# Performance work log

Measured on AMD Instinct MI355X. Metric: run time of the kernel, lower is better.

The kernel has to match this reference:

```python
import jax, jax.numpy as jnp
import numpy as np

G, N_PER, P_EDGE = 128, 20, 0.2
INPUT_DIM, HIDDEN, OUT_DIM = 32, 64, 10


def _build_structures():
    rng = np.random.default_rng(0)
    n, g = N_PER, G
    A = rng.random((g, n, n)) < P_EDGE
    A = np.triu(A, 1)
    A = A | A.transpose(0, 2, 1)  # symmetric, zero diag
    gi, uu, vv = np.nonzero(A)
    edge_index = np.stack([uu + gi * n, vv + gi * n]).astype(np.int64)
    batch = np.repeat(np.arange(g), n).astype(np.int64)
    # ---- 2-sets ----
    iu, ju = np.triu_indices(n, 1)
    P2 = len(iu)
    M2 = np.zeros((n, n), np.int64)
    M2[iu, ju] = np.arange(P2); M2[ju, iu] = np.arange(P2)
    gu2 = (np.arange(g)[:, None] * n + iu[None]).ravel().astype(np.int64)
    gv2 = (np.arange(g)[:, None] * n + ju[None]).ravel().astype(np.int64)
    iso2 = A[:, iu, ju].astype(np.float32).reshape(-1, 1)
    w = np.arange(n)
    # branch A: (u,v) -> (v,w) if adj[v,w] & w!=u & adj[u,w]; branch B symmetric
    condA = A[:, ju, :] & A[:, iu, :] & (w[None, None, :] != iu[None, :, None])
    condB = A[:, iu, :] & A[:, ju, :] & (w[None, None, :] != ju[None, :, None])
    ga_, ia_, wa_ = np.nonzero(condA)
    gb_, ib_, wb_ = np.nonzero(condB)
    src2 = np.concatenate([ia_ + ga_ * P2, ib_ + gb_ * P2])
    dst2 = np.concatenate([M2[ju[ia_], wa_] + ga_ * P2, M2[iu[ib_], wb_] + gb_ * P2])
    two_edges = np.stack([src2, dst2]).astype(np.int64)
    two_batch = np.repeat(np.arange(g), P2).astype(np.int64)
    # ---- 3-sets ----
    trips = np.array([(a, b, c) for a in range(n) for b in range(a + 1, n) for c in range(b + 1, n)], np.int64)
    a, b, c = trips[:, 0], trips[:, 1], trips[:, 2]
    P3 = len(trips)
    M3 = np.zeros((n, n, n), np.int64)
    M3[a, b, c] = np.arange(P3)
    ga3 = (np.arange(g)[:, None] * n + a[None]).ravel().astype(np.int64)
    gb3 = (np.arange(g)[:, None] * n + b[None]).ravel().astype(np.int64)
    gc3 = (np.arange(g)[:, None] * n + c[None]).ravel().astype(np.int64)
    ec = A[:, a, b].astype(np.int64) + A[:, b, c].astype(np.int64) + A[:, a, c].astype(np.int64)
    iso3 = np.eye(4, dtype=np.float32)[ec.reshape(-1)]
    notin = (w[None] != a[:, None]) & (w[None] != b[:, None]) & (w[None] != c[:, None])  # [P3,n]
    srcs, dsts = [], []
    # branches: replace c (keep a,b), replace b (keep a,c), replace a (keep b,c)
    for k0, k1, nbr in ((a, b, c), (a, c, b), (b, c, a)):
        cond = A[:, nbr, :] & notin[None]
        gg_, ii_, dd_ = np.nonzero(cond)
        tri = np.sort(np.stack([k0[ii_], k1[ii_], dd_], 1), 1)
        srcs.append(ii_ + gg_ * P3)
        dsts.append(M3[tri[:, 0], tri[:, 1], tri[:, 2]] + gg_ * P3)
    three_edges = np.stack([np.concatenate(srcs), np.concatenate(dsts)]).astype(np.int64)
    three_batch = np.repeat(np.arange(g), P3).astype(np.int64)
    x = rng.standard_normal((g * n, INPUT_DIM)).astype(np.float32)
    return (x, edge_index, batch, gu2, gv2, iso2, two_edges, two_batch,
            ga3, gb3, gc3, iso3, three_edges, three_batch)


def setup_inputs() -> dict:
    (x, edge_index, batch, gu2, gv2, iso2, two_edges, two_batch,
     ga3, gb3, gc3, iso3, three_edges, three_batch) = _build_structures()
    rw = np.random.default_rng(1)
    def W(o, i):
        return jnp.asarray((rw.standard_normal((o, i)) * 0.1).astype(np.float32))
    H = HIDDEN
    return dict(
        x=jnp.asarray(x), edge_index=jnp.asarray(edge_index), batch=jnp.asarray(batch),
        gu2=jnp.asarray(gu2), gv2=jnp.asarray(gv2), iso2=jnp.asarray(iso2),
        two_edges=jnp.asarray(two_edges), two_batch=jnp.asarray(two_batch),
        ga3=jnp.asarray(ga3), gb3=jnp.asarray(gb3), gc3=jnp.asarray(gc3),
        iso3=jnp.asarray(iso3), three_edges=jnp.asarray(three_edges),
        three_batch=jnp.asarray(three_batch),
        g1W1_0=W(H, INPUT_DIM), g1W2_0=W(H, INPUT_DIM),
        g1W1_1=W(H, H), g1W2_1=W(H, H), g1W1_2=W(H, H), g1W2_2=W(H, H),
        g2W1_0=W(H, 2 * H + 1), g2W2_0=W(H, 2 * H + 1), g2W1_1=W(H, H), g2W2_1=W(H, H),
        g3W1_0=W(H, 3 * H + 4), g3W2_0=W(H, 3 * H + 4), g3W1_1=W(H, H), g3W2_1=W(H, H),
        cW1=W(H, 3 * H), cb1=jnp.zeros((H,), jnp.float32),
        cW2=W(OUT_DIM, H), cb2=jnp.zeros((OUT_DIM,), jnp.float32),
    )


def _layer(h, W1, W2, src, dst, num):
    # f(s) = relu(h W1^T + scatter_add(h W2^T gathered at src, dst))
    msg = (h @ W2.T)[src]  # project-then-gather; same math as gather-then-project
    nb = jax.ops.segment_sum(msg, dst, num_segments=num)
    return jax.nn.relu(h @ W1.T + nb)


def reference(x, edge_index, batch, gu2, gv2, iso2, two_edges, two_batch,
              ga3, gb3, gc3, iso3, three_edges, three_batch,
              g1W1_0, g1W2_0, g1W1_1, g1W2_1, g1W1_2, g1W2_2,
              g2W1_0, g2W2_0, g2W1_1, g2W2_1,
              g3W1_0, g3W2_0, g3W1_1, g3W2_1,
              cW1, cb1, cW2, cb2):
    N = x.shape[0]
    h = x
    for W1, W2 in ((g1W1_0, g1W2_0), (g1W1_1, g1W2_1), (g1W1_2, g1W2_2)):
        h = _layer(h, W1, W2, edge_index[0], edge_index[1], N)
    emb1 = jax.ops.segment_sum(h, batch, num_segments=G)
    h2 = jnp.concatenate([h[gu2], h[gv2], iso2], axis=1)
    n2 = h2.shape[0]
    for W1, W2 in ((g2W1_0, g2W2_0), (g2W1_1, g2W2_1)):
        h2 = _layer(h2, W1, W2, two_edges[0], two_edges[1], n2)
    emb2 = jax.ops.segment_sum(h2, two_batch, num_segments=G)
    h3 = jnp.concatenate([h[ga3], h[gb3], h[gc3], iso3], axis=1)
    n3 = h3.shape[0]
    for W1, W2 in ((g3W1_0, g3W2_0), (g3W1_1, g3W2_1)):
        h3 = _layer(h3, W1, W2, three_edges[0], three_edges[1], n3)
    emb3 = jax.ops.segment_sum(h3, three_batch, num_segments=G)
    comb = jnp.concatenate([emb1, emb2, emb3], axis=1)
    hid = jax.nn.relu(comb @ cW1.T + cb1)  # dropout is identity in eval mode
    return hid @ cW2.T + cb2
```

## Files before the change

kernel.cpp:

```cpp
#include <hip/hip_runtime.h>
#include <hip/hip_bf16.h>

#define HID 64
#define MROWS 1140
#define PAD1 20
#define PAD2 40
#define PAD3 60

typedef __hip_bfloat16  bf16;
typedef __hip_bfloat162 bf162;
typedef unsigned short  u16;
typedef __attribute__((ext_vector_type(8))) short bf8v;
typedef __attribute__((ext_vector_type(4))) float f4v;
typedef __attribute__((ext_vector_type(4))) unsigned int u4v;
__device__ __forceinline__ float bl(bf16 h) { return __bfloat162float(h); }

__global__ void zero_k(int* p, int n) {
    int i = blockIdx.x * 256 + threadIdx.x;
    if (i < n) p[i] = 0;
}

__global__ void fillp_k(const int* e1, int E1, int* c1, u16* s1, int p1, int P1_,
                        const int* e2, int E2, int* c2, u16* s2, int p2, int P2_,
                        const int* e3, int E3, int* c3, u16* s3, int p3, int P3_,
                        int nb1, int nb2) {
    int b = blockIdx.x;
    const int* edges; int E; int* cur; u16* csrc; int pad; int P; int lb;
    if (b < nb1)            { edges = e1; E = E1; cur = c1; csrc = s1; pad = p1; P = P1_; lb = b; }
    else if (b < nb1 + nb2) { edges = e2; E = E2; cur = c2; csrc = s2; pad = p2; P = P2_; lb = b - nb1; }
    else                    { edges = e3; E = E3; cur = c3; csrc = s3; pad = p3; P = P3_; lb = b - nb1 - nb2; }
    int e = lb * 256 + threadIdx.x;
    if (e >= E) return;
    int d = edges[E + e];
    int slot = atomicAdd(&cur[d], 1);
    if (slot < pad) csrc[(size_t)d * pad + slot] = (u16)(edges[e] % P);
}

struct FJob {
    const float *W1t, *W2t;
    const int *ga, *gb, *gc;
    const float *iso;
    const float *wc1, *wc2; int ldw, isoC, nT;
    const float *Wl1, *Wl2;
    const u16 *csrc; const int *cnt; int pad;
    bf16 *zc; bf16 *m1g;
    int P, ntiles, comboff;
};

__device__ __forceinline__ int msw(int row, int ch) {
    return (row << 6) + ((ch ^ (row & 7)) << 3);
}
__device__ __forceinline__ void accu4(u4v v, float* f) {
#pragma unroll
    for (int i = 0; i < 4; ++i) {
        f[2 * i]     += __uint_as_float(v[i] << 16);
        f[2 * i + 1] += __uint_as_float(v[i] & 0xffff0000u);
    }
}
__device__ __forceinline__ void accxy4(u4v v, float* zx, float* zy) {
#pragma unroll
    for (int i = 0; i < 4; ++i) {
        zx[i] += __uint_as_float(v[i] << 16);
        zy[i] += __uint_as_float(v[i] & 0xffff0000u);
    }
}
__device__ __forceinline__ bf8v pack8(const float* f) {
    bf16 tmp[8];
#pragma unroll
    for (int e = 0; e < 8; ++e) tmp[e] = __float2bfloat16(f[e]);
    bf8v r; __builtin_memcpy(&r, tmp, 16); return r;
}
__device__ __forceinline__ bf8v pack8relu(const float* f) {
    bf16 tmp[8];
#pragma unroll
    for (int e = 0; e < 8; ++e) tmp[e] = __float2bfloat16(fmaxf(f[e], 0.f));
    bf8v r; __builtin_memcpy(&r, tmp, 16); return r;
}
__device__ __forceinline__ u4v asu4(bf8v v) { u4v r; __builtin_memcpy(&r, &v, 16); return r; }
__device__ __forceinline__ void hsacc(const bf162* tb, int nd, int c4, float* zx, float* zy) {
    u4v v0 = *(const u4v*)(tb + (nd << 6) + (((c4    ) ^ (nd & 15)) << 2));
    u4v v1 = *(const u4v*)(tb + (nd << 6) + (((c4 + 1) ^ (nd & 15)) << 2));
    accxy4(v0, zx, zy);
    accxy4(v1, zx + 4, zy + 4);
}
__device__ __forceinline__ void hsaccY(const bf162* tb, int nd, int c4, float* zy) {
    u4v v0 = *(const u4v*)(tb + (nd << 6) + (((c4    ) ^ (nd & 15)) << 2));
    u4v v1 = *(const u4v*)(tb + (nd << 6) + (((c4 + 1) ^ (nd & 15)) << 2));
#pragma unroll
    for (int i = 0; i < 4; ++i) {
        zy[i]     += __uint_as_float(v0[i] & 0xffff0000u);
        zy[4 + i] += __uint_as_float(v1[i] & 0xffff0000u);
    }
}
__device__ __forceinline__ void naccum(const bf16* mL, int nbr, int quad, float* acc) {
    u4v v0 = *(const u4v*)(mL + msw(nbr, quad));
    u4v v1 = *(const u4v*)(mL + msw(nbr, quad + 4));
    accu4(v0, acc); accu4(v1, acc + 8);
}

__device__ __forceinline__ void run_k1(const FJob& jb, int g, int h,
                                       bf16* mLDS, bf16* wstage, const float* hb) {
    int t = threadIdx.x;
    const int P = jb.P, nT = jb.nT;
    const int gbase = g * P, nb20 = g * 20;
    int lane = t & 63, wv = t >> 6, quad = lane >> 4, m16 = lane & 15;

    bf162* hsA = (bf162*)wstage;
    const bf162* hsB = hsA + 1280;
    const bf162* hsC = hsA + 2560;
    bf16* mW = mLDS;
    for (int i = t; i < nT * 8192; i += 1024) {
        int table = i >> 13, r = i & 8191;
        int e = r & 7, mm = (r >> 3) & 15, qq = (r >> 7) & 3;
        int kk = (r >> 9) & 1, mat = (r >> 10) & 1, nn = r >> 11;
        const float* W = mat ? jb.W2t : jb.W1t;
        mW[i] = __float2bfloat16(W[(size_t)(nn * 16 + mm) * jb.ldw + table * 64 + kk * 32 + qq * 8 + e]);
    }
    float* wcT = (float*)(wstage + 7680);
    if (t < 512) {
        int mat = t >> 8, c = (t >> 6) & 3, f = t & 63;
        const float* W = mat ? jb.wc2 : jb.wc1;
        wcT[mat * 256 + c * 64 + f] = (c < jb.isoC) ? W[f * jb.ldw + c] : 0.f;
    }
    __syncthreads();
    if (wv < nT) {
        const bf16* mWt = mW + wv * 8192;
        bf8v a[2][2];
#pragma unroll
        for (int rt = 0; rt < 2; ++rt) {
            int node = rt * 16 + m16;
#pragma unroll
            for (int kt = 0; kt < 2; ++kt) {
                float tmp[8] = {0.f, 0.f, 0.f, 0.f, 0.f, 0.f, 0.f, 0.f};
                if (node < 20) {
                    const float* hr = hb + node * 65 + kt * 32 + quad * 8;
#pragma unroll
                    for (int e = 0; e < 8; ++e) tmp[e] = hr[e];
                }
                a[rt][kt] = pack8(tmp);
            }
        }
        bf162* hsT = hsA + wv * 1280;
#pragma unroll
        for (int n = 0; n < 4; ++n) {
            const bf8v b1k0 = *(const bf8v*)(mWt + ((((n*2+0)*2+0)*4+quad)*16+m16)*8);
            const bf8v b1k1 = *(const bf8v*)(mWt + ((((n*2+0)*2+1)*4+quad)*16+m16)*8);
            const bf8v b2k0 = *(const bf8v*)(mWt + ((((n*2+1)*2+0)*4+quad)*16+m16)*8);
            const bf8v b2k1 = *(const bf8v*)(mWt + ((((n*2+1)*2+1)*4+quad)*16+m16)*8);
#pragma unroll
            for (int rt = 0; rt < 2; ++rt) {
                f4v acca = {0.f, 0.f, 0.f, 0.f};
                f4v accb = {0.f, 0.f, 0.f, 0.f};
                acca = __builtin_amdgcn_mfma_f32_16x16x32_bf16(a[rt][0], b1k0, acca, 0, 0, 0);
                acca = __builtin_amdgcn_mfma_f32_16x16x32_bf16(a[rt][1], b1k1, acca, 0, 0, 0);
                accb = __builtin_amdgcn_mfma_f32_16x16x32_bf16(a[rt][0], b2k0, accb, 0, 0, 0);
                accb = __builtin_amdgcn_mfma_f32_16x16x32_bf16(a[rt][1], b2k1, accb, 0, 0, 0);
                int col = n * 16 + m16, c4 = col >> 2;
#pragma unroll
                for (int r = 0; r < 4; ++r) {
                    int node = rt * 16 + quad * 4 + r;
                    if (node < 20) {
                        bf162 v; v.x = __float2bfloat16(acca[r]); v.y = __float2bfloat16(accb[r]);
                        hsT[(node << 6) + ((c4 ^ (node & 15)) << 2) + (col & 3)] = v;
                    }
                }
            }
        }
    }
    __syncthreads();

    bf8v z8[3][2];
#pragma unroll
    for (int k = 0; k < 3; ++k) {
        int tile = wv + k * 16;
        if (tile >= jb.ntiles) continue;
#pragma unroll
        for (int rt = 0; rt < 2; ++rt) {
            bool own = (rt == h);
            int row = tile * 32 + rt * 16 + m16;
            float zx[16], zy[16];
#pragma unroll
            for (int j = 0; j < 16; ++j) { zx[j] = 0.f; zy[j] = 0.f; }
            if (row < P) {
                size_t gr = (size_t)gbase + row;
                int na = jb.ga[gr] - nb20;
                int nb = jb.gb[gr] - nb20;
                int nc = 0;
                const float* w1r; const float* w2r; float isw;
                if (nT == 3) {
                    nc = jb.gc[gr] - nb20;
                    float4 iv = ((const float4*)jb.iso)[gr];
                    int ec = (int)(iv.y + 2.f * iv.z + 3.f * iv.w + 0.5f);
                    w1r = wcT + ec * 64; w2r = wcT + 256 + ec * 64; isw = 1.f;
                } else {
                    w1r = wcT; w2r = wcT + 256; isw = jb.iso[gr];
                }
#pragma unroll
                for (int kt = 0; kt < 2; ++kt) {
                    int c4 = kt * 8 + quad * 2;
                    int f0 = kt * 32 + quad * 8;
                    if (own) {
                        hsacc(hsA, na, c4, zx + kt * 8, zy + kt * 8);
                        hsacc(hsB, nb, c4, zx + kt * 8, zy + kt * 8);
                        if (nT == 3) hsacc(hsC, nc, c4, zx + kt * 8, zy + kt * 8);
#pragma unroll
                        for (int e = 0; e < 8; ++e)
                            zx[kt * 8 + e] = fmaf(isw, w1r[f0 + e], zx[kt * 8 + e]);
                    } else {
                        hsaccY(hsA, na, c4, zy + kt * 8);
                        hsaccY(hsB, nb, c4, zy + kt * 8);
                        if (nT == 3) hsaccY(hsC, nc, c4, zy + kt * 8);
                    }
#pragma unroll
                    for (int e = 0; e < 8; ++e)
                        zy[kt * 8 + e] = fmaf(isw, w2r[f0 + e], zy[kt * 8 + e]);
                }
                *(bf8v*)(mLDS + msw(row, quad))     = pack8(zy);
                *(bf8v*)(mLDS + msw(row, quad + 4)) = pack8(zy + 8);
            }
            if (own) { z8[k][0] = pack8(zx); z8[k][1] = pack8(zx + 8); }
        }
    }
    __syncthreads();

    for (int i = t; i < 8192; i += 1024) {
        int e = i & 7, mm = (i >> 3) & 15, qq = (i >> 7) & 3;
        int kk = (i >> 9) & 1, mat = (i >> 10) & 1, nn = i >> 11;
        const float* W = mat ? jb.Wl2 : jb.Wl1;
        wstage[i] = __float2bfloat16(W[(nn * 16 + mm) * HID + kk * 32 + qq * 8 + e]);
    }
#pragma unroll
    for (int k = 0; k < 3; ++k) {
        int tile = wv + k * 16;
        if (tile >= jb.ntiles) continue;
        int row = tile * 32 + h * 16 + m16;
        float acc[16];
#pragma unroll
        for (int j = 0; j < 16; ++j) acc[j] = 0.f;
        accu4(asu4(z8[k][0]), acc);
        accu4(asu4(z8[k][1]), acc + 8);
        if (row < P) {
            size_t gr = (size_t)gbase + row;
            int cnt = jb.cnt[gr];
            const u16* cs = jb.csrc + gr * (size_t)jb.pad;
            int kk = 0;
            for (; kk + 4 <= cnt; kk += 4) {
                int n0 = cs[kk], n1 = cs[kk + 1], n2 = cs[kk + 2], n3 = cs[kk + 3];
                naccum(mLDS, n0, quad, acc); naccum(mLDS, n1, quad, acc);
                naccum(mLDS, n2, quad, acc); naccum(mLDS, n3, quad, acc);
            }
            for (; kk < cnt; ++kk) naccum(mLDS, cs[kk], quad, acc);
        }
        z8[k][0] = pack8relu(acc);
        z8[k][1] = pack8relu(acc + 8);
    }
    __syncthreads();

#pragma unroll
    for (int k = 0; k < 3; ++k) {
        int tile = wv + k * 16;
        if (tile >= jb.ntiles) continue;
        int j0 = tile * 32;
#pragma unroll
        for (int n = 0; n < 4; ++n) {
            const bf8v b1k0 = *(const bf8v*)(wstage + ((((n*2+0)*2+0)*4+quad)*16+m16)*8);
            const bf8v b1k1 = *(const bf8v*)(wstage + ((((n*2+0)*2+1)*4+quad)*16+m16)*8);
            const bf8v b2k0 = *(const bf8v*)(wstage + ((((n*2+1)*2+0)*4+quad)*16+m16)*8);
            const bf8v b2k1 = *(const bf8v*)(wstage + ((((n*2+1)*2+1)*4+quad)*16+m16)*8);
            f4v acca = {0.f, 0.f, 0.f, 0.f};
            f4v accb = {0.f, 0.f, 0.f, 0.f};
            acca = __builtin_amdgcn_mfma_f32_16x16x32_bf16(z8[k][0], b1k0, acca, 0, 0, 0);
            acca = __builtin_amdgcn_mfma_f32_16x16x32_bf16(z8[k][1], b1k1, acca, 0, 0, 0);
            accb = __builtin_amdgcn_mfma_f32_16x16x32_bf16(z8[k][0], b2k0, accb, 0, 0, 0);
            accb = __builtin_amdgcn_mfma_f32_16x16x32_bf16(z8[k][1], b2k1, accb, 0, 0, 0);
            int col = n * 16 + m16;
#pragma unroll
            for (int r = 0; r < 4; ++r) {
                int row = j0 + h * 16 + quad * 4 + r;
                if (row < P) {
                    jb.zc[((size_t)gbase + row) * HID + col]  = __float2bfloat16(acca[r]);
                    jb.m1g[((size_t)gbase + row) * HID + col] = __float2bfloat16(accb[r]);
                }
            }
        }
    }
}

__global__ __launch_bounds__(1024, 1)
void fused23a_k(const float* __restrict__ x,
                const int* __restrict__ cnt1, const u16* __restrict__ csrc1,
                const float* __restrict__ W10, const float* __restrict__ W20,
                const float* __restrict__ W11, const float* __restrict__ W21,
                const float* __restrict__ W12, const float* __restrict__ W22,
                FJob j3, FJob j2, float* __restrict__ comb, int G) {
    __shared__ __align__(16) bf16 mLDS[MROWS * HID];
    __shared__ __align__(16) bf16 wstage[8768];
    int b = blockIdx.x, t = threadIdx.x;
    int g = b >> 1, h = b & 1;
    if (h == 0 && t < 128) comb[g * 192 + 64 + t] = 0.f;

    float* hb = (float*)(mLDS + 70360);
    float* mb = (float*)(mLDS + 67800);
    float* zb = (float*)(mLDS + 65240);
    bf16* wf  = mLDS;
    int lane = t & 63, wv = t >> 6, quad = lane >> 4, m16 = lane & 15;
    int col = lane, r0 = wv;
    bool has2 = r0 < 4; int r1 = 16 + r0;
    if (t < 640) hb[(t >> 5) * 65 + (t & 31)] = x[(size_t)g * 640 + t];
    for (int i = t; i < 20480; i += 1024) {
        bf16 v;
        if (i < 4096) {
            int r = i;
            int e = r & 7, mm = (r >> 3) & 15, qq = (r >> 7) & 3;
            int mat = (r >> 9) & 1, nn = r >> 10;
            const float* W = mat ? W20 : W10;
            v = __float2bfloat16(W[(nn * 16 + mm) * 32 + qq * 8 + e]);
        } else {
            int j = i - 4096;
            int l2 = j >> 13, r = j & 8191;
            int e = r & 7, mm = (r >> 3) & 15, qq = (r >> 7) & 3;
            int kt = (r >> 9) & 1, mat = (r >> 10) & 1, nn = r >> 11;
            const float* W = l2 ? (mat ? W22 : W12) : (mat ? W21 : W11);
            v = __float2bfloat16(W[(nn * 16 + mm) * 64 + kt * 32 + qq * 8 + e]);
        }
        wf[i] = v;
    }
    __syncthreads();
#pragma unroll 1
    for (int l = 0; l < 3; ++l) {
        if (wv < 2) {
            const bf16* wbase = wf + (l == 0 ? 0 : (l == 1 ? 4096 : 12288));
            const int nK = l ? 2 : 1;
            const int lstep = l ? 2048 : 1024;
            const int mstep = l ? 1024 : 512;
            bf8v a[2][2];
#pragma unroll
            for (int rt = 0; rt < 2; ++rt) {
                int node = rt * 16 + m16;
#pragma unroll
                for (int kt = 0; kt < 2; ++kt) {
                    float tmp[8] = {0.f, 0.f, 0.f, 0.f, 0.f, 0.f, 0.f, 0.f};
                    if (node < 20 && kt < nK) {
                        const float* hr = hb + node * 65 + kt * 32 + quad * 8;
#pragma unroll
                        for (int e = 0; e < 8; ++e) tmp[e] = hr[e];
                    }
                    a[rt][kt] = pack8(tmp);
                }
            }
            float* ob = wv ? mb : zb;
#pragma unroll
            for (int n = 0; n < 4; ++n) {
                const bf16* bp = wbase + n * lstep + wv * mstep + (quad * 16 + m16) * 8;
                bf8v b0 = *(const bf8v*)bp;
                bf8v b1 = b0;
                if (l) b1 = *(const bf8v*)(bp + 512);
#pragma unroll
                for (int rt = 0; rt < 2; ++rt) {
                    f4v acc = {0.f, 0.f, 0.f, 0.f};
                    acc = __builtin_amdgcn_mfma_f32_16x16x32_bf16(a[rt][0], b0, acc, 0, 0, 0);
                    if (l) acc = __builtin_amdgcn_mfma_f32_16x16x32_bf16(a[rt][1], b1, acc, 0, 0, 0);
                    int c = n * 16 + m16;
#pragma unroll
                    for (int r = 0; r < 4; ++r) {
                        int row = rt * 16 + quad * 4 + r;
                        if (row < 20) ob[row * 64 + c] = acc[r];
                    }
                }
            }
        }
        __syncthreads();
        {
            float az = zb[r0 * 64 + col];
            int cnt = cnt1[g * 20 + r0];
            const u16* cs = csrc1 + (size_t)(g * 20 + r0) * PAD1;
            for (int k = 0; k < cnt; ++k) az += mb[cs[k] * 64 + col];
            hb[r0 * 65 + col] = fmaxf(az, 0.f);
        }
        if (has2) {
            float az = zb[r1 * 64 + col];
            int cnt = cnt1[g * 20 + r1];
            const u16* cs = csrc1 + (size_t)(g * 20 + r1) * PAD1;
            for (int k = 0; k < cnt; ++k) az += mb[cs[k] * 64 + col];
            hb[r1 * 65 + col] = fmaxf(az, 0.f);
        }
        __syncthreads();
    }
    if (h == 0 && t < 64) {
        float s = 0.f;
#pragma unroll
        for (int r = 0; r < 20; ++r) s += hb[r * 65 + t];
        comb[g * 192 + t] = s;
    }
    run_k1(j2, g, h, mLDS, wstage, hb);
    __syncthreads();
    run_k1(j3, g, h, mLDS, wstage, hb);
}

__device__ __forceinline__ void run_k2(const FJob& jb, int g, int h,
                                       bf16* mLDS, float* part, float* comb) {
    int t = threadIdx.x;
    const int P = jb.P;
    const int gbase = g * P;
    int lane = t & 63, wv = t >> 6, quad = lane >> 4, m16 = lane & 15;
    for (int i = t; i < P * 8; i += 1024) {
        int row = i >> 3, ch = i & 7;
        u4v v = *(const u4v*)(jb.m1g + ((size_t)gbase + row) * HID + ch * 8);
        *(u4v*)(mLDS + msw(row, ch)) = v;
    }
    __syncthreads();
    float ps[16];
#pragma unroll
    for (int j = 0; j < 16; ++j) ps[j] = 0.f;
#pragma unroll
    for (int k = 0; k < 3; ++k) {
        int tile = wv + k * 16;
        if (tile >= jb.ntiles) continue;
        int row = tile * 32 + h * 16 + m16;
        if (row < P) {
            float acc[16];
#pragma unroll
            for (int j = 0; j < 16; ++j) acc[j] = 0.f;
            size_t gr = (size_t)gbase + row;
            u4v zc0 = *(const u4v*)(jb.zc + gr * HID + quad * 8);
            u4v zc1 = *(const u4v*)(jb.zc + gr * HID + 32 + quad * 8);
            accu4(zc0, acc); accu4(zc1, acc + 8);
            int cnt = jb.cnt[gr];
            const u16* cs = jb.csrc + gr * (size_t)jb.pad;
            int kk = 0;
            for (; kk + 4 <= cnt; kk += 4) {
                int n0 = cs[kk], n1 = cs[kk + 1], n2 = cs[kk + 2], n3 = cs[kk + 3];
                naccum(mLDS, n0, quad, acc); naccum(mLDS, n1, quad, acc);
                naccum(mLDS, n2, quad, acc); naccum(mLDS, n3, quad, acc);
            }
            for (; kk < cnt; ++kk) naccum(mLDS, cs[kk], quad, acc);
#pragma unroll
            for (int j = 0; j < 16; ++j) ps[j] += fmaxf(acc[j], 0.f);
        }
    }
#pragma unroll
    for (int j = 0; j < 16; ++j) {
        ps[j] += __shfl_xor(ps[j], 1, 64);
        ps[j] += __shfl_xor(ps[j], 2, 64);
        ps[j] += __shfl_xor(ps[j], 4, 64);
        ps[j] += __shfl_xor(ps[j], 8, 64);
    }
    if (m16 == 0) {
#pragma unroll
        for (int kt = 0; kt < 2; ++kt)
#pragma unroll
            for (int e = 0; e < 8; ++e)
                part[wv * 64 + kt * 32 + quad * 8 + e] = ps[kt * 8 + e];
    }
    __syncthreads();
    if (t < 64) {
        float s = 0.f;
#pragma unroll
        for (int w = 0; w < 16; ++w) s += part[w * 64 + t];
        atomicAdd(&comb[g * 192 + jb.comboff + t], s);
    }
    __syncthreads();
}

__global__ __launch_bounds__(1024, 1)
void fused23b_k(FJob j3, FJob j2, float* __restrict__ comb, int G) {
    __shared__ __align__(16) bf16 mLDS[MROWS * HID];
    __shared__ float part[1024];
    int b = blockIdx.x;
    int g = b >> 1, h = b & 1;
    run_k2(j3, g, h, mLDS, part, comb);
    run_k2(j2, g, h, mLDS, part, comb);
}

__global__ void classifier_k(const float* __restrict__ comb,
                             const float* __restrict__ cW1, const float* __restrict__ cb1,
                             const float* __restrict__ cW2, const float* __restrict__ cb2,
                             float* __restrict__ out) {
    __shared__ float row[192];
    __shared__ float hid[64];
    int g = blockIdx.x, t = threadIdx.x;
    for (int i = t; i < 192; i += 64) row[i] = comb[g * 192 + i];
    __syncthreads();
    float acc = cb1[t];
#pragma unroll 8
    for (int k = 0; k < 192; ++k) acc += row[k] * cW1[t * 192 + k];
    hid[t] = fmaxf(acc, 0.f);
    __syncthreads();
    if (t < 10) {
        float o = cb2[t];
#pragma unroll
        for (int k = 0; k < 64; ++k) o += hid[k] * cW2[t * 64 + k];
        out[g * 10 + t] = o;
    }
}

static inline int cdiv(long long a, long long b) { return (int)((a + b - 1) / b); }

extern "C" void kernel_launch(void* const* d_in, const int* in_sizes, int n_in,
                              void* d_out, int out_size, void* d_ws, size_t ws_size,
                              hipStream_t stream) {
    const float* x        = (const float*)d_in[0];
    const int*   eidx     = (const int*)d_in[1];
    const int*   gu2      = (const int*)d_in[3];
    const int*   gv2      = (const int*)d_in[4];
    const float* iso2     = (const float*)d_in[5];
    const int*   tedges   = (const int*)d_in[6];
    const int*   ga3      = (const int*)d_in[8];
    const int*   gb3      = (const int*)d_in[9];
    const int*   gc3      = (const int*)d_in[10];
    const float* iso3     = (const float*)d_in[11];
    const int*   hedges   = (const int*)d_in[12];
    const float* g1W1[3]  = {(const float*)d_in[14], (const float*)d_in[16], (const float*)d_in[18]};
    const float* g1W2[3]  = {(const float*)d_in[15], (const float*)d_in[17], (const float*)d_in[19]};
    const float* g2W1_0   = (const float*)d_in[20];
    const float* g2W2_0   = (const float*)d_in[21];
    const float* g2W1_1   = (const float*)d_in[22];
    const float* g2W2_1   = (const float*)d_in[23];
    const float* g3W1_0   = (const float*)d_in[24];
    const float* g3W2_0   = (const float*)d_in[25];
    const float* g3W1_1   = (const float*)d_in[26];
    const float* g3W2_1   = (const float*)d_in[27];
    const float* cW1      = (const float*)d_in[28];
    const float* cb1      = (const float*)d_in[29];
    const float* cW2      = (const float*)d_in[30];
    const float* cb2      = (const float*)d_in[31];
    float* out = (float*)d_out;

    const int N  = in_sizes[0] / 32;
    const int E1 = in_sizes[1] / 2;
    const int n2 = in_sizes[3];
    const int E2 = in_sizes[6] / 2;
    const int n3 = in_sizes[8];
    const int E3 = in_sizes[12] / 2;
    const int G  = out_size / 10;
    const int per1 = N / G, per2 = n2 / G, per3 = n3 / G;

    float* ws = (float*)d_ws;
    size_t off = 0;
    auto alloc = [&](size_t n) { off = (off + 3) & ~(size_t)3; float* p = ws + off; off += n; return p; };
    bf16* z2c = (bf16*)alloc((size_t)n2 * HID / 2 + 64);
    bf16* z3c = (bf16*)alloc((size_t)n3 * HID / 2 + 64);
    bf16* m2g = (bf16*)alloc((size_t)n2 * HID / 2 + 64);
    bf16* m3g = (bf16*)alloc((size_t)n3 * HID / 2 + 64);
    float* comb = alloc((size_t)G * 192);
    int* iws = (int*)(ws + off);
    size_t ioff = 0;
    auto ialloc = [&](size_t n) { int* p = iws + ioff; ioff += n; return p; };
    int* cur1 = ialloc(N); int* cur2 = ialloc(n2); int* cur3 = ialloc(n3);
    u16* u16ws = (u16*)(iws + ioff);
    size_t uoff = 0;
    auto ualloc = [&](size_t n) { u16* p = u16ws + uoff; uoff += n; return p; };
    u16* csrc1 = ualloc((size_t)N * PAD1);
    u16* csrc2 = ualloc((size_t)n2 * PAD2);
    u16* csrc3 = ualloc((size_t)n3 * PAD3);
    (void)ws_size;

    dim3 B256(256);

    int ncnt = N + n2 + n3;
    zero_k<<<cdiv(ncnt, 256), B256, 0, stream>>>(cur1, ncnt);
    int ne1 = cdiv(E1, 256), ne2 = cdiv(E2, 256), ne3 = cdiv(E3, 256);
    fillp_k<<<ne1 + ne2 + ne3, B256, 0, stream>>>(
        eidx, E1, cur1, csrc1, PAD1, per1,
        tedges, E2, cur2, csrc2, PAD2, per2,
        hedges, E3, cur3, csrc3, PAD3, per3, ne1, ne2);

    {
        FJob j3, j2;
        j3.W1t = g3W1_0; j3.W2t = g3W2_0;
        j3.ga = ga3; j3.gb = gb3; j3.gc = gc3;
        j3.iso = iso3; j3.wc1 = g3W1_0 + 192; j3.wc2 = g3W2_0 + 192;
        j3.ldw = 196; j3.isoC = 4; j3.nT = 3;
        j3.Wl1 = g3W1_1; j3.Wl2 = g3W2_1;
        j3.csrc = csrc3; j3.cnt = cur3; j3.pad = PAD3;
        j3.zc = z3c; j3.m1g = m3g;
        j3.P = per3; j3.ntiles = (per3 + 31) >> 5; j3.comboff = 128;

        j2.W1t = g2W1_0; j2.W2t = g2W2_0;
        j2.ga = gu2; j2.gb = gv2; j2.gc = nullptr;
        j2.iso = iso2; j2.wc1 = g2W1_0 + 128; j2.wc2 = g2W2_0 + 128;
        j2.ldw = 129; j2.isoC = 1; j2.nT = 2;
        j2.Wl1 = g2W1_1; j2.Wl2 = g2W2_1;
        j2.csrc = csrc2; j2.cnt = cur2; j2.pad = PAD2;
        j2.zc = z2c; j2.m1g = m2g;
        j2.P = per2; j2.ntiles = (per2 + 31) >> 5; j2.comboff = 64;

        fused23a_k<<<2 * G, 1024, 0, stream>>>(x, cur1, csrc1,
            g1W1[0], g1W2[0], g1W1[1], g1W2[1], g1W1[2], g1W2[2], j3, j2, comb, G);
        fused23b_k<<<2 * G, 1024, 0, stream>>>(j3, j2, comb, G);
    }

    classifier_k<<<G, 64, 0, stream>>>(comb, cW1, cb1, cW2, cb2, out);
}
```

Before: 256.9 us.

## Fuse second GNN layer into first kernel with redundant full-row computation per block

Each block of a pair now computes the first-layer message for both row halves, so it holds every row's m1 value in LDS. That lets it run the second layer's neighbor aggregation in the same kernel, which removes the m1g global round-trip and the separate fused23b launch. The comb zeroing moves into the combined zero kernel. In exchange, each block does twice the layer-1 aggregation and MFMA work for the W2 path and keeps more register state (z8 doubled), which could reduce throughput.

Result: slower. 275.0 us (+7.0%).

```diff
diff --git a/kernel.cpp b/kernel.cpp
--- a/kernel.cpp
+++ b/kernel.cpp
@@ -15,9 +15,10 @@
 typedef __attribute__((ext_vector_type(4))) unsigned int u4v;
 __device__ __forceinline__ float bl(bf16 h) { return __bfloat162float(h); }
 
-__global__ void zero_k(int* p, int n) {
-    int i = blockIdx.x * 256 + threadIdx.x;
-    if (i < n) p[i] = 0;
+__global__ void zero2_k(int* p1, int n1, int* p2, int n2, int nb1) {
+    int b = blockIdx.x;
+    if (b < nb1) { int i = b * 256 + threadIdx.x; if (i < n1) p1[i] = 0; }
+    else { int i = (b - nb1) * 256 + threadIdx.x; if (i < n2) p2[i] = 0; }
 }
 
 __global__ void fillp_k(const int* e1, int E1, int* c1, u16* s1, int p1, int P1_,
@@ -43,7 +44,7 @@
     const float *wc1, *wc2; int ldw, isoC, nT;
     const float *Wl1, *Wl2;
     const u16 *csrc; const int *cnt; int pad;
-    bf16 *zc; bf16 *m1g;
+    bf16 *zc;
     int P, ntiles, comboff;
 };
 
@@ -83,23 +84,15 @@
     accxy4(v0, zx, zy);
     accxy4(v1, zx + 4, zy + 4);
 }
-__device__ __forceinline__ void hsaccY(const bf162* tb, int nd, int c4, float* zy) {
-    u4v v0 = *(const u4v*)(tb + (nd << 6) + (((c4    ) ^ (nd & 15)) << 2));
-    u4v v1 = *(const u4v*)(tb + (nd << 6) + (((c4 + 1) ^ (nd & 15)) << 2));
-#pragma unroll
-    for (int i = 0; i < 4; ++i) {
-        zy[i]     += __uint_as_float(v0[i] & 0xffff0000u);
-        zy[4 + i] += __uint_as_float(v1[i] & 0xffff0000u);
-    }
-}
 __device__ __forceinline__ void naccum(const bf16* mL, int nbr, int quad, float* acc) {
     u4v v0 = *(const u4v*)(mL + msw(nbr, quad));
     u4v v1 = *(const u4v*)(mL + msw(nbr, quad + 4));
     accu4(v0, acc); accu4(v1, acc + 8);
 }
 
-__device__ __forceinline__ void run_k1(const FJob& jb, int g, int h,
-                                       bf16* mLDS, bf16* wstage, const float* hb) {
+__device__ __forceinline__ void run_level(const FJob& jb, int g, int h,
+                                          bf16* mLDS, bf16* wstage, const float* hb,
+                                          float* comb) {
     int t = threadIdx.x;
     const int P = jb.P, nT = jb.nT;
     const int gbase = g * P, nb20 = g * 20;
@@ -169,14 +162,13 @@
     }
     __syncthreads();
 
-    bf8v z8[3][2];
+    bf8v z8[3][2][2];
 #pragma unroll
     for (int k = 0; k < 3; ++k) {
         int tile = wv + k * 16;
         if (tile >= jb.ntiles) continue;
 #pragma unroll
         for (int rt = 0; rt < 2; ++rt) {
-            bool own = (rt == h);
             int row = tile * 32 + rt * 16 + m16;
             float zx[16], zy[16];
 #pragma unroll
@@ -199,26 +191,20 @@
                 for (int kt = 0; kt < 2; ++kt) {
                     int c4 = kt * 8 + quad * 2;
                     int f0 = kt * 32 + quad * 8;
-                    if (own) {
-                        hsacc(hsA, na, c4, zx + kt * 8, zy + kt * 8);
-                        hsacc(hsB, nb, c4, zx + kt * 8, zy + kt * 8);
-                        if (nT == 3) hsacc(hsC, nc, c4, zx + kt * 8, zy + kt * 8);
-#pragma unroll
-                        for (int e = 0; e < 8; ++e)
-                            zx[kt * 8 + e] = fmaf(isw, w1r[f0 + e], zx[kt * 8 + e]);
-                    } else {
-                        hsaccY(hsA, na, c4, zy + kt * 8);
-                        hsaccY(hsB, nb, c4, zy + kt * 8);
-                        if (nT == 3) hsaccY(hsC, nc, c4, zy + kt * 8);
+                    hsacc(hsA, na, c4, zx + kt * 8, zy + kt * 8);
+                    hsacc(hsB, nb, c4, zx + kt * 8, zy + kt * 8);
+                    if (nT == 3) hsacc(hsC, nc, c4, zx + kt * 8, zy + kt * 8);
+#pragma unroll
+                    for (int e = 0; e < 8; ++e) {
+                        zx[kt * 8 + e] = fmaf(isw, w1r[f0 + e], zx[kt * 8 + e]);
+                        zy[kt * 8 + e] = fmaf(isw, w2r[f0 + e], zy[kt * 8 + e]);
                     }
-#pragma unroll
-                    for (int e = 0; e < 8; ++e)
-                        zy[kt * 8 + e] = fmaf(isw, w2r[f0 + e], zy[kt * 8 + e]);
                 }
                 *(bf8v*)(mLDS + msw(row, quad))     = pack8(zy);
                 *(bf8v*)(mLDS + msw(row, quad + 4)) = pack8(zy + 8);
             }
-            if (own) { z8[k][0] = pack8(zx); z8[k][1] = pack8(zx + 8); }
+            z8[k][rt][0] = pack8(zx);
+            z8[k][rt][1] = pack8(zx + 8);
         }
     }
     __syncthreads();
@@ -233,14 +219,87 @@
     for (int k = 0; k < 3; ++k) {
         int tile = wv + k * 16;
         if (tile >= jb.ntiles) continue;
+#pragma unroll
+        for (int rt = 0; rt < 2; ++rt) {
+            int row = tile * 32 + rt * 16 + m16;
+            float acc[16];
+#pragma unroll
+            for (int j = 0; j < 16; ++j) acc[j] = 0.f;
+            accu4(asu4(z8[k][rt][0]), acc);
+            accu4(asu4(z8[k][rt][1]), acc + 8);
+            if (row < P) {
+                size_t gr = (size_t)gbase + row;
+                int cnt = jb.cnt[gr];
+                const u16* cs = jb.csrc + gr * (size_t)jb.pad;
+                int kk = 0;
+                for (; kk + 4 <= cnt; kk += 4) {
+                    int n0 = cs[kk], n1 = cs[kk + 1], n2 = cs[kk + 2], n3 = cs[kk + 3];
+                    naccum(mLDS, n0, quad, acc); naccum(mLDS, n1, quad, acc);
+                    naccum(mLDS, n2, quad, acc); naccum(mLDS, n3, quad, acc);
+                }
+                for (; kk < cnt; ++kk) naccum(mLDS, cs[kk], quad, acc);
+            }
+            z8[k][rt][0] = pack8relu(acc);
+            z8[k][rt][1] = pack8relu(acc + 8);
+        }
+    }
+    __syncthreads();
+
+#pragma unroll
+    for (int k = 0; k < 3; ++k) {
+        int tile = wv + k * 16;
+        if (tile >= jb.ntiles) continue;
+        int j0 = tile * 32;
+#pragma unroll
+        for (int n = 0; n < 4; ++n) {
+            const bf8v b1k0 = *(const bf8v*)(wstage + ((((n*2+0)*2+0)*4+quad)*16+m16)*8);
+            const bf8v b1k1 = *(const bf8v*)(wstage + ((((n*2+0)*2+1)*4+quad)*16+m16)*8);
+            const bf8v b2k0 = *(const bf8v*)(wstage + ((((n*2+1)*2+0)*4+quad)*16+m16)*8);
+            const bf8v b2k1 = *(const bf8v*)(wstage + ((((n*2+1)*2+1)*4+quad)*16+m16)*8);
+            int col = n * 16 + m16, ch = col >> 3, ce = col & 7;
+#pragma unroll
+            for (int rt = 0; rt < 2; ++rt) {
+                f4v accb = {0.f, 0.f, 0.f, 0.f};
+                accb = __builtin_amdgcn_mfma_f32_16x16x32_bf16(z8[k][rt][0], b2k0, accb, 0, 0, 0);
+                accb = __builtin_amdgcn_mfma_f32_16x16x32_bf16(z8[k][rt][1], b2k1, accb, 0, 0, 0);
+                if (rt == h) {
+                    f4v acca = {0.f, 0.f, 0.f, 0.f};
+                    acca = __builtin_amdgcn_mfma_f32_16x16x32_bf16(z8[k][rt][0], b1k0, acca, 0, 0, 0);
+                    acca = __builtin_amdgcn_mfma_f32_16x16x32_bf16(z8[k][rt][1], b1k1, acca, 0, 0, 0);
+#pragma unroll
+                    for (int r = 0; r < 4; ++r) {
+                        int row = j0 + rt * 16 + quad * 4 + r;
+                        if (row < P)
+                            jb.zc[((size_t)gbase + row) * HID + col] = __float2bfloat16(acca[r]);
+                    }
+                }
+#pragma unroll
+                for (int r = 0; r < 4; ++r) {
+                    int row = j0 + rt * 16 + quad * 4 + r;
+                    if (row < P)
+                        mLDS[(row << 6) + ((ch ^ (row & 7)) << 3) + ce] = __float2bfloat16(accb[r]);
+                }
+            }
+        }
+    }
+    __syncthreads();
+
+    float ps[16];
+#pragma unroll
+    for (int j = 0; j < 16; ++j) ps[j] = 0.f;
+#pragma unroll
+    for (int k = 0; k < 3; ++k) {
+        int tile = wv + k * 16;
+        if (tile >= jb.ntiles) continue;
         int row = tile * 32 + h * 16 + m16;
-        float acc[16];
-#pragma unroll
-        for (int j = 0; j < 16; ++j) acc[j] = 0.f;
-        accu4(asu4(z8[k][0]), acc);
-        accu4(asu4(z8[k][1]), acc + 8);
         if (row < P) {
+            float acc[16];
+#pragma unroll
+            for (int j = 0; j < 16; ++j) acc[j] = 0.f;
             size_t gr = (size_t)gbase + row;
+            u4v zc0 = *(const u4v*)(jb.zc + gr * HID + quad * 8);
+            u4v zc1 = *(const u4v*)(jb.zc + gr * HID + 32 + quad * 8);
+            accu4(zc0, acc); accu4(zc1, acc + 8);
             int cnt = jb.cnt[gr];
             const u16* cs = jb.csrc + gr * (size_t)jb.pad;
             int kk = 0;
@@ -250,40 +309,33 @@
                 naccum(mLDS, n2, quad, acc); naccum(mLDS, n3, quad, acc);
             }
             for (; kk < cnt; ++kk) naccum(mLDS, cs[kk], quad, acc);
-        }
-        z8[k][0] = pack8relu(acc);
-        z8[k][1] = pack8relu(acc + 8);
-    }
-    __syncthreads();
-
-#pragma unroll
-    for (int k = 0; k < 3; ++k) {
-        int tile = wv + k * 16;
-        if (tile >= jb.ntiles) continue;
-        int j0 = tile * 32;
-#pragma unroll
-        for (int n = 0; n < 4; ++n) {
-            const bf8v b1k0 = *(const bf8v*)(wstage + ((((n*2+0)*2+0)*4+quad)*16+m16)*8);
-            const bf8v b1k1 = *(const bf8v*)(wstage + ((((n*2+0)*2+1)*4+quad)*16+m16)*8);
-            const bf8v b2k0 = *(const bf8v*)(wstage + ((((n*2+1)*2+0)*4+quad)*16+m16)*8);
-            const bf8v b2k1 = *(const bf8v*)(wstage + ((((n*2+1)*2+1)*4+quad)*16+m16)*8);
-            f4v acca = {0.f, 0.f, 0.f, 0.f};
-            f4v accb = {0.f, 0.f, 0.f, 0.f};
-            acca = __builtin_amdgcn_mfma_f32_16x16x32_bf16(z8[k][0], b1k0, acca, 0, 0, 0);
-            acca = __builtin_amdgcn_mfma_f32_16x16x32_bf16(z8[k][1], b1k1, acca, 0, 0, 0);
-            accb = __builtin_amdgcn_mfma_f32_16x16x32_bf16(z8[k][0], b2k0, accb, 0, 0, 0);
-            accb = __builtin_amdgcn_mfma_f32_16x16x32_bf16(z8[k][1], b2k1, accb, 0, 0, 0);
-            int col = n * 16 + m16;
-#pragma unroll
-            for (int r = 0; r < 4; ++r) {
-                int row = j0 + h * 16 + quad * 4 + r;
-                if (row < P) {
-                    jb.zc[((size_t)gbase + row) * HID + col]  = __float2bfloat16(acca[r]);
-                    jb.m1g[((size_t)gbase + row) * HID + col] = __float2bfloat16(accb[r]);
-                }
-            }
-        }
-    }
+#pragma unroll
+            for (int j = 0; j < 16; ++j) ps[j] += fmaxf(acc[j], 0.f);
+        }
+    }
+#pragma unroll
+    for (int j = 0; j < 16; ++j) {
+        ps[j] += __shfl_xor(ps[j], 1, 64);
+        ps[j] += __shfl_xor(ps[j], 2, 64);
+        ps[j] += __shfl_xor(ps[j], 4, 64);
+        ps[j] += __shfl_xor(ps[j], 8, 64);
+    }
+    float* part = (float*)wstage;
+    if (m16 == 0) {
+#pragma unroll
+        for (int kt = 0; kt < 2; ++kt)
+#pragma unroll
+            for (int e = 0; e < 8; ++e)
+                part[wv * 64 + kt * 32 + quad * 8 + e] = ps[kt * 8 + e];
+    }
+    __syncthreads();
+    if (t < 64) {
+        float s = 0.f;
+#pragma unroll
+        for (int w = 0; w < 16; ++w) s += part[w * 64 + t];
+        atomicAdd(&comb[g * 192 + jb.comboff + t], s);
+    }
+    __syncthreads();
 }
 
 __global__ __launch_bounds__(1024, 1)
@@ -297,7 +349,6 @@
     __shared__ __align__(16) bf16 wstage[8768];
     int b = blockIdx.x, t = threadIdx.x;
     int g = b >> 1, h = b & 1;
-    if (h == 0 && t < 128) comb[g * 192 + 64 + t] = 0.f;
 
     float* hb = (float*)(mLDS + 70360);
     float* mb = (float*)(mLDS + 67800);
@@ -392,84 +443,9 @@
         for (int r = 0; r < 20; ++r) s += hb[r * 65 + t];
         comb[g * 192 + t] = s;
     }
-    run_k1(j2, g, h, mLDS, wstage, hb);
-    __syncthreads();
-    run_k1(j3, g, h, mLDS, wstage, hb);
-}
-
-__device__ __forceinline__ void run_k2(const FJob& jb, int g, int h,
-                                       bf16* mLDS, float* part, float* comb) {
-    int t = threadIdx.x;
-    const int P = jb.P;
-    const int gbase = g * P;
-    int lane = t & 63, wv = t >> 6, quad = lane >> 4, m16 = lane & 15;
-    for (int i = t; i < P * 8; i += 1024) {
-        int row = i >> 3, ch = i & 7;
-        u4v v = *(const u4v*)(jb.m1g + ((size_t)gbase + row) * HID + ch * 8);
-        *(u4v*)(mLDS + msw(row, ch)) = v;
-    }
-    __syncthreads();
-    float ps[16];
-#pragma unroll
-    for (int j = 0; j < 16; ++j) ps[j] = 0.f;
-#pragma unroll
-    for (int k = 0; k < 3; ++k) {
-        int tile = wv + k * 16;
-        if (tile >= jb.ntiles) continue;
-        int row = tile * 32 + h * 16 + m16;
-        if (row < P) {
-            float acc[16];
-#pragma unroll
-            for (int j = 0; j < 16; ++j) acc[j] = 0.f;
-            size_t gr = (size_t)gbase + row;
-            u4v zc0 = *(const u4v*)(jb.zc + gr * HID + quad * 8);
-            u4v zc1 = *(const u4v*)(jb.zc + gr * HID + 32 + quad * 8);
-            accu4(zc0, acc); accu4(zc1, acc + 8);
-            int cnt = jb.cnt[gr];
-            const u16* cs = jb.csrc + gr * (size_t)jb.pad;
-            int kk = 0;
-            for (; kk + 4 <= cnt; kk += 4) {
-                int n0 = cs[kk], n1 = cs[kk + 1], n2 = cs[kk + 2], n3 = cs[kk + 3];
-                naccum(mLDS, n0, quad, acc); naccum(mLDS, n1, quad, acc);
-                naccum(mLDS, n2, quad, acc); naccum(mLDS, n3, quad, acc);
-            }
-            for (; kk < cnt; ++kk) naccum(mLDS, cs[kk], quad, acc);
-#pragma unroll
-            for (int j = 0; j < 16; ++j) ps[j] += fmaxf(acc[j], 0.f);
-        }
-    }
-#pragma unroll
-    for (int j = 0; j < 16; ++j) {
-        ps[j] += __shfl_xor(ps[j], 1, 64);
-        ps[j] += __shfl_xor(ps[j], 2, 64);
-        ps[j] += __shfl_xor(ps[j], 4, 64);
-        ps[j] += __shfl_xor(ps[j], 8, 64);
-    }
-    if (m16 == 0) {
-#pragma unroll
-        for (int kt = 0; kt < 2; ++kt)
-#pragma unroll
-            for (int e = 0; e < 8; ++e)
-                part[wv * 64 + kt * 32 + quad * 8 + e] = ps[kt * 8 + e];
-    }
-    __syncthreads();
-    if (t < 64) {
-        float s = 0.f;
-#pragma unroll
-        for (int w = 0; w < 16; ++w) s += part[w * 64 + t];
-        atomicAdd(&comb[g * 192 + jb.comboff + t], s);
-    }
-    __syncthreads();
-}
-
-__global__ __launch_bounds__(1024, 1)
-void fused23b_k(FJob j3, FJob j2, float* __restrict__ comb, int G) {
-    __shared__ __align__(16) bf16 mLDS[MROWS * HID];
-    __shared__ float part[1024];
-    int b = blockIdx.x;
-    int g = b >> 1, h = b & 1;
-    run_k2(j3, g, h, mLDS, part, comb);
-    run_k2(j2, g, h, mLDS, part, comb);
+    run_level(j2, g, h, mLDS, wstage, hb, comb);
+    __syncthreads();
+    run_level(j3, g, h, mLDS, wstage, hb, comb);
 }
 
 __global__ void classifier_k(const float* __restrict__ comb,
@@ -540,8 +516,6 @@
     auto alloc = [&](size_t n) { off = (off + 3) & ~(size_t)3; float* p = ws + off; off += n; return p; };
     bf16* z2c = (bf16*)alloc((size_t)n2 * HID / 2 + 64);
     bf16* z3c = (bf16*)alloc((size_t)n3 * HID / 2 + 64);
-    bf16* m2g = (bf16*)alloc((size_t)n2 * HID / 2 + 64);
-    bf16* m3g = (bf16*)alloc((size_t)n3 * HID / 2 + 64);
     float* comb = alloc((size_t)G * 192);
     int* iws = (int*)(ws + off);
     size_t ioff = 0;
@@ -558,7 +532,8 @@
     dim3 B256(256);
 
     int ncnt = N + n2 + n3;
-    zero_k<<<cdiv(ncnt, 256), B256, 0, stream>>>(cur1, ncnt);
+    int nbc = cdiv(ncnt, 256), nbz = cdiv(G * 192, 256);
+    zero2_k<<<nbc + nbz, B256, 0, stream>>>(cur1, ncnt, (int*)comb, G * 192, nbc);
     int ne1 = cdiv(E1, 256), ne2 = cdiv(E2, 256), ne3 = cdiv(E3, 256);
     fillp_k<<<ne1 + ne2 + ne3, B256, 0, stream>>>(
         eidx, E1, cur1, csrc1, PAD1, per1,
@@ -573,7 +548,7 @@
         j3.ldw = 196; j3.isoC = 4; j3.nT = 3;
         j3.Wl1 = g3W1_1; j3.Wl2 = g3W2_1;
         j3.csrc = csrc3; j3.cnt = cur3; j3.pad = PAD3;
-        j3.zc = z3c; j3.m1g = m3g;
+        j3.zc = z3c;
         j3.P = per3; j3.ntiles = (per3 + 31) >> 5; j3.comboff = 128;
 
         j2.W1t = g2W1_0; j2.W2t = g2W2_0;
@@ -582,12 +557,11 @@
         j2.ldw = 129; j2.isoC = 1; j2.nT = 2;
         j2.Wl1 = g2W1_1; j2.Wl2 = g2W2_1;
         j2.csrc = csrc2; j2.cnt = cur2; j2.pad = PAD2;
-        j2.zc = z2c; j2.m1g = m2g;
+        j2.zc = z2c;
         j2.P = per2; j2.ntiles = (per2 + 31) >> 5; j2.comboff = 64;
 
         fused23a_k<<<2 * G, 1024, 0, stream>>>(x, cur1, csrc1,
             g1W1[0], g1W2[0], g1W1[1], g1W2[1], g1W1[2], g1W2[2], j3, j2, comb, G);
-        fused23b_k<<<2 * G, 1024, 0, stream>>>(j3, j2, comb, G);
     }
 
     classifier_k<<<G, 64, 0, stream>>>(comb, cW1, cb1, cW2, cb2, out);
```
